# Optimization experiments

Measured on AMD Instinct MI355X. Metric: run time of the kernel, lower is better.

The kernel has to match this reference:

```python
import jax, jax.numpy as jnp
import numpy as np

N, S, D = 8, 1024, 512      # batch, seq_len, in_dim
H, KD, VD, OD = 8, 64, 64, 512  # heads, key_dim, value_dim, out_dim
GRAPH_WEIGHT = 0.5
NEG_INF = float('-inf')


def setup_inputs() -> dict:
    key = jax.random.key(0)
    ks = jax.random.split(key, 9)
    return {
        "x":    jax.random.normal(ks[0], (N, S, D), jnp.float32),
        "Wk":   jax.random.normal(ks[1], (H, D, KD), jnp.float32) * 0.02,
        "bk":   jax.random.normal(ks[2], (H, KD), jnp.float32) * 0.02,
        "Wv":   jax.random.normal(ks[3], (H, D, VD), jnp.float32) * 0.02,
        "bv":   jax.random.normal(ks[4], (H, VD), jnp.float32) * 0.02,
        "Wout": jax.random.normal(ks[5], (H * VD, OD), jnp.float32) * 0.02,
        "bout": jax.random.normal(ks[6], (OD,), jnp.float32) * 0.02,
        "graph": jax.random.normal(ks[7], (S, S), jnp.float32),
        "knn": 64,
    }


def reference(x, Wk, bk, Wv, bv, Wout, bout, graph, knn):
    # Per-head key/value projections (heads vectorized on leading axis h).
    k = jnp.einsum('nsd,hdk->hnsk', x, Wk) + bk[:, None, None, :]   # (H,N,S,KD)
    v = jnp.einsum('nsd,hdv->hnsv', x, Wv) + bv[:, None, None, :]   # (H,N,S,VD)
    q = k  # self-attention: query = key

    # att_unnorm = (q . k) / sqrt(key_dim)  -> (H,N,S,S)
    att = jnp.einsum('hnqk,hntk->hnqt', q, k) / np.sqrt(KD).astype(np.float32)

    # Causal mask (equivalent to the Python loop att[:, i, i+1:] = -inf).
    causal = jnp.tril(jnp.ones((S, S), dtype=bool))
    att = jnp.where(causal, att, NEG_INF)

    # knn top-k pooling: keep top-knn entries along the last axis, rest -> -inf.
    topv = jax.lax.top_k(att, knn)[0]                  # (H,N,S,knn)
    kth = topv[..., -1:]                               # kth largest per row
    att = jnp.where(att >= kth, att, NEG_INF)

    p = jax.nn.softmax(att, axis=-1)

    # Graph-weighted attention blend (graph is row-softmaxed at init time).
    att_graph = jax.nn.softmax(graph, axis=-1)         # (S,S)
    p = GRAPH_WEIGHT * att_graph + (1.0 - GRAPH_WEIGHT) * p

    # y_h = att @ value, then concat heads and output projection.
    y = jnp.einsum('hnqt,hntv->hnqv', p, v)            # (H,N,S,VD)
    y = y.transpose(1, 2, 0, 3).reshape(N, S, H * VD)  # head-major concat
    return y @ Wout + bout
```

## Files before the change

kernel.cpp:

```cpp
#include <hip/hip_runtime.h>
#include <math.h>

#define NB 8
#define SL 1024
#define DI 512
#define HH 8
#define KDN 64
#define VDN 64
#define ODN 512
#define ATT_SCALE 0.125f

#define KLO_OFF 2097152u
#define V_OFF   4194304u
#define G_OFF   8388608u
#define Y_OFF   9437184u

#define ORD_NEG_INF 0x007FFFFFu

typedef __attribute__((ext_vector_type(8))) short bf16x8;
typedef __attribute__((ext_vector_type(4))) float f32x4;

__device__ __forceinline__ unsigned fordu(float f) {
  unsigned b = __float_as_uint(f);
  return b ^ ((b & 0x80000000u) ? 0xFFFFFFFFu : 0x80000000u);
}
__device__ __forceinline__ float ifordu(unsigned k) {
  unsigned b = k ^ ((k & 0x80000000u) ? 0x80000000u : 0xFFFFFFFFu);
  return __uint_as_float(b);
}
__device__ __forceinline__ unsigned short f2bf(float f) {
  unsigned u = __float_as_uint(f);
  unsigned r = (u + 0x7FFFu + ((u >> 16) & 1u)) >> 16;
  return (unsigned short)r;
}
__device__ __forceinline__ float bf2f(unsigned short h) {
  return __uint_as_float(((unsigned)h) << 16);
}

__global__ __launch_bounds__(256) void kvproj_kernel(
    const float* __restrict__ x, const float* __restrict__ Wk, const float* __restrict__ bk,
    const float* __restrict__ Wv, const float* __restrict__ bv, float* __restrict__ ws)
{
  __shared__ float xs[64][68];
  __shared__ float wks[64][68];
  __shared__ float wvs[64][68];
  const int tid = threadIdx.x;
  const int tx = tid & 15, ty = tid >> 4;
  const int m0 = blockIdx.x * 64;
  const int h = blockIdx.y;
  const float* wkb = Wk + (size_t)h * (DI * KDN);
  const float* wvb = Wv + (size_t)h * (DI * VDN);
  float ak[4][4] = {{0.f}};
  float av[4][4] = {{0.f}};
  for (int dt = 0; dt < DI / 64; ++dt) {
    __syncthreads();
#pragma unroll
    for (int it = 0; it < 4; ++it) {
      const int r = ty + it * 16;
      const int c = tx * 4;
      *(float4*)&xs[r][c]  = *(const float4*)&x[(size_t)(m0 + r) * DI + dt * 64 + c];
      *(float4*)&wks[r][c] = *(const float4*)&wkb[(size_t)(dt * 64 + r) * KDN + c];
      *(float4*)&wvs[r][c] = *(const float4*)&wvb[(size_t)(dt * 64 + r) * VDN + c];
    }
    __syncthreads();
#pragma unroll 4
    for (int dd = 0; dd < 64; ++dd) {
      float a[4];
#pragma unroll
      for (int i = 0; i < 4; ++i) a[i] = xs[ty * 4 + i][dd];
      const float4 bkv = *(const float4*)&wks[dd][tx * 4];
      const float4 bvv = *(const float4*)&wvs[dd][tx * 4];
      const float bkj[4] = {bkv.x, bkv.y, bkv.z, bkv.w};
      const float bvj[4] = {bvv.x, bvv.y, bvv.z, bvv.w};
#pragma unroll
      for (int i = 0; i < 4; ++i) {
#pragma unroll
        for (int j = 0; j < 4; ++j) {
          ak[i][j] = __fmaf_rn(a[i], bkj[j], ak[i][j]);
          av[i][j] = __fmaf_rn(a[i], bvj[j], av[i][j]);
        }
      }
    }
  }
  const int n = m0 >> 10;
  const int s0 = m0 & 1023;
  float* vb = ws + V_OFF;
  unsigned short* khi = (unsigned short*)ws;
  unsigned short* klo = (unsigned short*)(ws + KLO_OFF);
#pragma unroll
  for (int i = 0; i < 4; ++i) {
    const int s = s0 + ty * 4 + i;
    float4 vv;
    vv.x = av[i][0] + bv[h * VDN + tx * 4 + 0];
    vv.y = av[i][1] + bv[h * VDN + tx * 4 + 1];
    vv.z = av[i][2] + bv[h * VDN + tx * 4 + 2];
    vv.w = av[i][3] + bv[h * VDN + tx * 4 + 3];
    *(float4*)&vb[((size_t)(h * NB + n) * SL + s) * VDN + tx * 4] = vv;
    union { unsigned short u[4]; uint2 v2; } ph, pl;
#pragma unroll
    for (int j = 0; j < 4; ++j) {
      const float kf = ak[i][j] + bk[h * KDN + tx * 4 + j];
      const unsigned short h16 = f2bf(kf);
      ph.u[j] = h16;
      pl.u[j] = f2bf(kf - bf2f(h16));
    }
    const size_t koff = ((size_t)(h * NB + n) * SL + s) * KDN + tx * 4;
    *(uint2*)&khi[koff] = ph.v2;
    *(uint2*)&klo[koff] = pl.v2;
  }
}

__global__ __launch_bounds__(256) void gsoftmax_kernel(const float* __restrict__ gin, float* __restrict__ ws)
{
  float* gout = ws + G_OFF;
  const int row = blockIdx.x;
  const int tid = threadIdx.x;
  const int lane = tid & 63, wave = tid >> 6;
  __shared__ float red[4];
  __shared__ float red2[4];
  float v[4];
  float m = -INFINITY;
#pragma unroll
  for (int i = 0; i < 4; ++i) {
    v[i] = gin[(size_t)row * SL + tid + i * 256];
    m = fmaxf(m, v[i]);
  }
#pragma unroll
  for (int off = 32; off; off >>= 1) m = fmaxf(m, __shfl_xor(m, off));
  if (lane == 0) red[wave] = m;
  __syncthreads();
  m = fmaxf(fmaxf(red[0], red[1]), fmaxf(red[2], red[3]));
  float e[4];
  float s = 0.f;
#pragma unroll
  for (int i = 0; i < 4; ++i) { e[i] = __expf(v[i] - m); s += e[i]; }
#pragma unroll
  for (int off = 32; off; off >>= 1) s += __shfl_xor(s, off);
  if (lane == 0) red2[wave] = s;
  __syncthreads();
  s = red2[0] + red2[1] + red2[2] + red2[3];
  const float inv = 1.0f / s;
#pragma unroll
  for (int i = 0; i < 4; ++i) gout[(size_t)row * SL + tid + i * 256] = e[i] * inv;
}

__global__ __launch_bounds__(256, 4) void attn_kernel(float* __restrict__ ws, const int* __restrict__ knn_p)
{
  __shared__ float S[16][260];
  const int tid = threadIdx.x;
  const int lane = tid & 63;
  const int wave = tid >> 6;
  const int q0 = blockIdx.x * 16;
  const int hn = blockIdx.y;
  const int h = hn >> 3, n = hn & 7;
  const int K = knn_p[0];
  const unsigned short* khi = (const unsigned short*)ws + (size_t)hn * SL * KDN;
  const unsigned short* klo = (const unsigned short*)(ws + KLO_OFF) + (size_t)hn * SL * KDN;
  const float* vb = ws + V_OFF + (size_t)hn * (SL * VDN);
  float* y = ws + Y_OFF;

  const int col = lane & 15, grp = lane >> 4;
  const bf16x8 a0h = *(const bf16x8*)&khi[(size_t)(q0 + col) * KDN + grp * 8];
  const bf16x8 a1h = *(const bf16x8*)&khi[(size_t)(q0 + col) * KDN + 32 + grp * 8];
  const bf16x8 a0l = *(const bf16x8*)&klo[(size_t)(q0 + col) * KDN + grp * 8];
  const bf16x8 a1l = *(const bf16x8*)&klo[(size_t)(q0 + col) * KDN + 32 + grp * 8];

  const int T = q0 / 16 + 1;
  const int rbase = wave * 4;

  float ev[4][8][2];
#pragma unroll
  for (int rr = 0; rr < 4; ++rr)
#pragma unroll
    for (int c = 0; c < 8; ++c) {
      ev[rr][c][0] = __uint_as_float(ORD_NEG_INF);
      ev[rr][c][1] = __uint_as_float(ORD_NEG_INF);
    }

#pragma unroll
  for (int ph = 0; ph < 4; ++ph) {
    const int tlo = ph * 16;
    const int thi = (T < tlo + 16) ? T : (tlo + 16);
    if (thi > tlo) {
      __syncthreads();
      for (int ti = tlo + wave; ti < thi; ti += 4) {
        const int t0 = ti * 16;
        const size_t bo = (size_t)(t0 + col) * KDN + grp * 8;
        const bf16x8 b0h = *(const bf16x8*)&khi[bo];
        const bf16x8 b1h = *(const bf16x8*)&khi[bo + 32];
        const bf16x8 b0l = *(const bf16x8*)&klo[bo];
        const bf16x8 b1l = *(const bf16x8*)&klo[bo + 32];
        f32x4 d = {0.f, 0.f, 0.f, 0.f};
        d = __builtin_amdgcn_mfma_f32_16x16x32_bf16(a0h, b0h, d, 0, 0, 0);
        d = __builtin_amdgcn_mfma_f32_16x16x32_bf16(a1h, b1h, d, 0, 0, 0);
        d = __builtin_amdgcn_mfma_f32_16x16x32_bf16(a0h, b0l, d, 0, 0, 0);
        d = __builtin_amdgcn_mfma_f32_16x16x32_bf16(a1h, b1l, d, 0, 0, 0);
        d = __builtin_amdgcn_mfma_f32_16x16x32_bf16(a0l, b0h, d, 0, 0, 0);
        d = __builtin_amdgcn_mfma_f32_16x16x32_bf16(a1l, b1h, d, 0, 0, 0);
        d = __builtin_amdgcn_mfma_f32_16x16x32_bf16(a0l, b0l, d, 0, 0, 0);
        d = __builtin_amdgcn_mfma_f32_16x16x32_bf16(a1l, b1l, d, 0, 0, 0);
        const int tl = t0 - ph * 256 + col;
#pragma unroll
        for (int r = 0; r < 4; ++r) S[grp * 4 + r][tl] = d[r];
      }
      __syncthreads();
#pragma unroll
      for (int rr = 0; rr < 4; ++rr) {
        const int q = q0 + rbase + rr;
        const int cmr = q >> 7;
#pragma unroll
        for (int cc = 0; cc < 2; ++cc) {
          const int c = ph * 2 + cc;
          if (c <= cmr) {
            const float2 sv = *(const float2*)&S[rbase + rr][cc * 128 + lane * 2];
            const int t0 = c * 128 + lane * 2;
            const unsigned k0 = (t0     <= q) ? fordu(sv.x * ATT_SCALE) : ORD_NEG_INF;
            const unsigned k1 = (t0 + 1 <= q) ? fordu(sv.y * ATT_SCALE) : ORD_NEG_INF;
            ev[rr][c][0] = __uint_as_float(k0);
            ev[rr][c][1] = __uint_as_float(k1);
          }
        }
      }
    }
  }
  __syncthreads();

  float* elist = (float*)((char*)&S[0][0] + wave * 768);
  unsigned short* tlist = (unsigned short*)(elist + 128);

#pragma unroll
  for (int rr = 0; rr < 4; ++rr) {
    const int q = q0 + rbase + rr;

    unsigned u[16];
#pragma unroll
    for (int c = 0; c < 8; ++c) {
      u[c * 2]     = __float_as_uint(ev[rr][c][0]);
      u[c * 2 + 1] = __float_as_uint(ev[rr][c][1]);
    }

    unsigned lmax = u[0];
#pragma unroll
    for (int i = 1; i < 16; ++i) lmax = lmax > u[i] ? lmax : u[i];
    unsigned mk = lmax, t0k = lmax;
#pragma unroll
    for (int off = 32; off; off >>= 1) {
      const unsigned om = (unsigned)__shfl_xor((int)mk, off);
      const unsigned ot = (unsigned)__shfl_xor((int)t0k, off);
      mk = mk > om ? mk : om;
      t0k = t0k < ot ? t0k : ot;
    }
    const float m = ifordu(mk);

    unsigned kth;
    if (q < K) {
      kth = ORD_NEG_INF;
    } else {
      unsigned lo = (K <= 64) ? t0k : 0u;
      unsigned hi = mk;
      while (lo < hi) {
        const unsigned mid = lo + ((hi - lo + 1) >> 1);
        int cnt = 0;
#pragma unroll
        for (int i = 0; i < 16; ++i)
          cnt += (int)__popcll(__ballot(u[i] >= mid));
        if (cnt >= K) lo = mid; else hi = mid - 1;
      }
      kth = lo;
    }

    float Z = 0.f;
#pragma unroll
    for (int c = 0; c < 8; ++c) {
#pragma unroll
      for (int j = 0; j < 2; ++j) {
        const unsigned k = u[c * 2 + j];
        float e = 0.f;
        if (k >= kth) e = __expf(ifordu(k) - m);
        ev[rr][c][j] = e;
        Z += e;
      }
    }
#pragma unroll
    for (int off = 32; off; off >>= 1) Z += __shfl_xor(Z, off);

    const unsigned long long lt = (1ull << lane) - 1ull;
    int cnt = 0;
#pragma unroll
    for (int c = 0; c < 8; ++c) {
#pragma unroll
      for (int j = 0; j < 2; ++j) {
        const float e = ev[rr][c][j];
        const unsigned long long msk = __ballot(e > 0.f);
        if (e > 0.f) {
          const int pos = cnt + (int)__popcll(msk & lt);
          if (pos < 128) {
            elist[pos] = e;
            tlist[pos] = (unsigned short)(c * 128 + lane * 2 + j);
          }
        }
        cnt += (int)__popcll(msk);
      }
    }
    cnt = (cnt < 128) ? cnt : 128;

    float yacc = 0.f;
    int i2 = 0;
    for (; i2 + 4 <= cnt; i2 += 4) {
      const float4 e4 = *(const float4*)&elist[i2];
      const ushort4 t4 = *(const ushort4*)&tlist[i2];
      yacc = __fmaf_rn(e4.x, vb[(size_t)t4.x * VDN + lane], yacc);
      yacc = __fmaf_rn(e4.y, vb[(size_t)t4.y * VDN + lane], yacc);
      yacc = __fmaf_rn(e4.z, vb[(size_t)t4.z * VDN + lane], yacc);
      yacc = __fmaf_rn(e4.w, vb[(size_t)t4.w * VDN + lane], yacc);
    }
    for (; i2 < cnt; ++i2) {
      yacc = __fmaf_rn(elist[i2], vb[(size_t)tlist[i2] * VDN + lane], yacc);
    }
    y[((size_t)(n * SL + q)) * ODN + h * VDN + lane] = yacc * (0.5f / Z);
  }
}

__global__ __launch_bounds__(256) void gv_kernel(float* __restrict__ ws)
{
  __shared__ float as_[64][68];
  __shared__ float bs_[64][68];
  const int tid = threadIdx.x;
  const int tx = tid & 15, ty = tid >> 4;
  const int q0 = blockIdx.x * 64;
  const int hn = blockIdx.y;
  const int h = hn >> 3, n = hn & 7;
  const float* g = ws + G_OFF;
  const float* vb = ws + V_OFF + (size_t)hn * (SL * VDN);
  float* y = ws + Y_OFF;
  float acc[4][4] = {{0.f}};
  for (int kt = 0; kt < 16; ++kt) {
    __syncthreads();
#pragma unroll
    for (int it = 0; it < 4; ++it) {
      const int r = ty + it * 16;
      const int c = tx * 4;
      *(float4*)&as_[r][c] = *(const float4*)&g[(size_t)(q0 + r) * SL + kt * 64 + c];
      *(float4*)&bs_[r][c] = *(const float4*)&vb[(size_t)(kt * 64 + r) * VDN + c];
    }
    __syncthreads();
#pragma unroll 4
    for (int dd = 0; dd < 64; ++dd) {
      float a[4];
#pragma unroll
      for (int i = 0; i < 4; ++i) a[i] = as_[ty * 4 + i][dd];
      const float4 b4 = *(const float4*)&bs_[dd][tx * 4];
      const float bj[4] = {b4.x, b4.y, b4.z, b4.w};
#pragma unroll
      for (int i = 0; i < 4; ++i)
#pragma unroll
        for (int j = 0; j < 4; ++j)
          acc[i][j] = __fmaf_rn(a[i], bj[j], acc[i][j]);
    }
  }
#pragma unroll
  for (int i = 0; i < 4; ++i) {
    const size_t off = ((size_t)(n * SL + q0 + ty * 4 + i)) * ODN + h * VDN + tx * 4;
    float4 cur = *(float4*)&y[off];
    cur.x += 0.5f * acc[i][0];
    cur.y += 0.5f * acc[i][1];
    cur.z += 0.5f * acc[i][2];
    cur.w += 0.5f * acc[i][3];
    *(float4*)&y[off] = cur;
  }
}

__global__ __launch_bounds__(256) void wtprep_kernel(const float* __restrict__ Wout, float* __restrict__ ws)
{
  __shared__ float tile[64][65];
  unsigned short* wth = (unsigned short*)ws;
  unsigned short* wtl = wth + ODN * ODN;
  const int t = threadIdx.x;
  const int od0 = blockIdx.x * 64;
  const int k0 = blockIdx.y * 64;
  const int r = t >> 2, c4 = (t & 3) * 16;
#pragma unroll
  for (int j = 0; j < 4; ++j) {
    *(float4*)&tile[r][c4 + j * 4] = *(const float4*)&Wout[(size_t)(k0 + r) * ODN + od0 + c4 + j * 4];
  }
  __syncthreads();
  union { unsigned short u[16]; uint4 v[2]; } hi, lo;
#pragma unroll
  for (int j = 0; j < 16; ++j) {
    const float f = tile[c4 + j][r];
    const unsigned short h16 = f2bf(f);
    hi.u[j] = h16;
    lo.u[j] = f2bf(f - bf2f(h16));
  }
  const size_t o = (size_t)(od0 + r) * ODN + k0 + c4;
  *(uint4*)&wth[o] = hi.v[0];
  *(uint4*)&wth[o + 8] = hi.v[1];
  *(uint4*)&wtl[o] = lo.v[0];
  *(uint4*)&wtl[o + 8] = lo.v[1];
}

__global__ __launch_bounds__(256) void out_kernel(
    const float* __restrict__ bout, const float* __restrict__ ws, float* __restrict__ out)
{
  const unsigned short* wth = (const unsigned short*)ws;
  const unsigned short* wtl = wth + ODN * ODN;
  const float* y = ws + Y_OFF;
  const int tid = threadIdx.x;
  const int lane = tid & 63;
  const int wave = tid >> 6;
  const int col = lane & 15, grp = lane >> 4;
  const int od0 = blockIdx.x * 64;
  const int m0 = blockIdx.y * 64 + wave * 16;

  f32x4 acc[4];
#pragma unroll
  for (int odt = 0; odt < 4; ++odt) acc[odt] = (f32x4){0.f, 0.f, 0.f, 0.f};

  const float* yrow = y + (size_t)(m0 + col) * ODN + grp * 8;
  for (int ks = 0; ks < 16; ++ks) {
    const float4 ya = *(const float4*)&yrow[ks * 32];
    const float4 yb = *(const float4*)&yrow[ks * 32 + 4];
    union { unsigned short u[8]; bf16x8 v; } ah, al;
    const float yf[8] = {ya.x, ya.y, ya.z, ya.w, yb.x, yb.y, yb.z, yb.w};
#pragma unroll
    for (int j = 0; j < 8; ++j) {
      const unsigned short h16 = f2bf(yf[j]);
      ah.u[j] = h16;
      al.u[j] = f2bf(yf[j] - bf2f(h16));
    }
#pragma unroll
    for (int odt = 0; odt < 4; ++odt) {
      const size_t bo = (size_t)(od0 + odt * 16 + col) * ODN + ks * 32 + grp * 8;
      const bf16x8 bh = *(const bf16x8*)&wth[bo];
      const bf16x8 bl = *(const bf16x8*)&wtl[bo];
      acc[odt] = __builtin_amdgcn_mfma_f32_16x16x32_bf16(ah.v, bh, acc[odt], 0, 0, 0);
      acc[odt] = __builtin_amdgcn_mfma_f32_16x16x32_bf16(ah.v, bl, acc[odt], 0, 0, 0);
      acc[odt] = __builtin_amdgcn_mfma_f32_16x16x32_bf16(al.v, bh, acc[odt], 0, 0, 0);
    }
  }

#pragma unroll
  for (int odt = 0; odt < 4; ++odt) {
    const int od = od0 + odt * 16 + col;
    const float bo = bout[od];
#pragma unroll
    for (int r = 0; r < 4; ++r) {
      out[(size_t)(m0 + grp * 4 + r) * ODN + od] = acc[odt][r] + bo;
    }
  }
}

extern "C" void kernel_launch(void* const* d_in, const int* in_sizes, int n_in,
                              void* d_out, int out_size, void* d_ws, size_t ws_size,
                              hipStream_t stream)
{
  const float* x     = (const float*)d_in[0];
  const float* Wk    = (const float*)d_in[1];
  const float* bk    = (const float*)d_in[2];
  const float* Wv    = (const float*)d_in[3];
  const float* bv    = (const float*)d_in[4];
  const float* Wout  = (const float*)d_in[5];
  const float* bout  = (const float*)d_in[6];
  const float* graph = (const float*)d_in[7];
  const int*   knn   = (const int*)d_in[8];
  float* out = (float*)d_out;
  float* ws  = (float*)d_ws;

  kvproj_kernel<<<dim3(128, 8), 256, 0, stream>>>(x, Wk, bk, Wv, bv, ws);
  gsoftmax_kernel<<<dim3(1024), 256, 0, stream>>>(graph, ws);
  attn_kernel<<<dim3(64, 64), 256, 0, stream>>>(ws, knn);
  wtprep_kernel<<<dim3(8, 8), 256, 0, stream>>>(Wout, ws);
  gv_kernel<<<dim3(16, 64), 256, 0, stream>>>(ws);
  out_kernel<<<dim3(8, 128), 256, 0, stream>>>(bout, ws, out);
}
```

Before: 604.0 us.

## Move KV projection and graph-value GEMM to split-bf16 MFMA

The fp32 scalar-FMA GEMMs in kvproj and gv are replaced with bf16x3 split-precision MFMA (hi*hi + hi*lo + lo*hi). New prep kernels split x, Wk/Wv, the graph softmax and a transposed V into hi/lo bf16 halves, and workspace regions are reused and remapped, with wtprep moved after gv. The aim is to use matrix cores for these GEMMs in exchange for extra launches, conversion traffic and slightly lower precision. Output stores become scalar, and LDS tiling is dropped in favour of direct global loads.

```diff
diff --git a/kernel.cpp b/kernel.cpp
--- a/kernel.cpp
+++ b/kernel.cpp
@@ -37,82 +37,124 @@
   return __uint_as_float(((unsigned)h) << 16);
 }
 
+__global__ __launch_bounds__(256) void xprep_kernel(const float* __restrict__ x, float* __restrict__ ws)
+{
+  unsigned short* xhi = (unsigned short*)(ws + Y_OFF);
+  unsigned short* xlo = xhi + (size_t)NB * SL * DI;
+  const size_t i = (size_t)blockIdx.x * 256 + threadIdx.x;
+  const float4 v = *(const float4*)&x[i * 4];
+  const float vf[4] = {v.x, v.y, v.z, v.w};
+  union { unsigned short u[4]; uint2 v2; } hi, lo;
+#pragma unroll
+  for (int j = 0; j < 4; ++j) {
+    const unsigned short h16 = f2bf(vf[j]);
+    hi.u[j] = h16;
+    lo.u[j] = f2bf(vf[j] - bf2f(h16));
+  }
+  *(uint2*)&xhi[i * 4] = hi.v2;
+  *(uint2*)&xlo[i * 4] = lo.v2;
+}
+
+__global__ __launch_bounds__(256) void wprep_kernel(
+    const float* __restrict__ Wk, const float* __restrict__ Wv, float* __restrict__ ws)
+{
+  __shared__ float tile[64][65];
+  unsigned short* gbase = (unsigned short*)(ws + G_OFF);
+  const int t = threadIdx.x;
+  const int d0 = blockIdx.x * 64;
+  const int hs = blockIdx.y;
+  const int h = hs & 7, which = hs >> 3;
+  const float* W = (which == 0) ? (Wk + (size_t)h * DI * KDN) : (Wv + (size_t)h * DI * VDN);
+  unsigned short* whi = gbase + (size_t)which * 524288 + (size_t)h * KDN * DI;
+  unsigned short* wlo = whi + 262144;
+  const int r = t >> 2, c4 = (t & 3) * 16;
+#pragma unroll
+  for (int j = 0; j < 4; ++j)
+    *(float4*)&tile[r][c4 + j * 4] = *(const float4*)&W[(size_t)(d0 + r) * KDN + c4 + j * 4];
+  __syncthreads();
+  union { unsigned short u[16]; uint4 v[2]; } hi, lo;
+#pragma unroll
+  for (int j = 0; j < 16; ++j) {
+    const float f = tile[c4 + j][r];
+    const unsigned short h16 = f2bf(f);
+    hi.u[j] = h16;
+    lo.u[j] = f2bf(f - bf2f(h16));
+  }
+  const size_t o = (size_t)r * DI + d0 + c4;
+  *(uint4*)&whi[o] = hi.v[0];
+  *(uint4*)&whi[o + 8] = hi.v[1];
+  *(uint4*)&wlo[o] = lo.v[0];
+  *(uint4*)&wlo[o + 8] = lo.v[1];
+}
+
 __global__ __launch_bounds__(256) void kvproj_kernel(
-    const float* __restrict__ x, const float* __restrict__ Wk, const float* __restrict__ bk,
-    const float* __restrict__ Wv, const float* __restrict__ bv, float* __restrict__ ws)
-{
-  __shared__ float xs[64][68];
-  __shared__ float wks[64][68];
-  __shared__ float wvs[64][68];
+    const float* __restrict__ bk, const float* __restrict__ bv, float* __restrict__ ws)
+{
+  const unsigned short* xhi = (const unsigned short*)(ws + Y_OFF);
+  const unsigned short* xlo = xhi + (size_t)NB * SL * DI;
+  const unsigned short* gbase = (const unsigned short*)(ws + G_OFF);
+  const unsigned short* wkthi = gbase;
+  const unsigned short* wktlo = gbase + 262144;
+  const unsigned short* wvthi = gbase + 524288;
+  const unsigned short* wvtlo = gbase + 786432;
+  unsigned short* khi = (unsigned short*)ws;
+  unsigned short* klo = (unsigned short*)(ws + KLO_OFF);
+  float* vb = ws + V_OFF;
+
   const int tid = threadIdx.x;
-  const int tx = tid & 15, ty = tid >> 4;
+  const int lane = tid & 63;
+  const int wave = tid >> 6;
+  const int col = lane & 15, grp = lane >> 4;
   const int m0 = blockIdx.x * 64;
   const int h = blockIdx.y;
-  const float* wkb = Wk + (size_t)h * (DI * KDN);
-  const float* wvb = Wv + (size_t)h * (DI * VDN);
-  float ak[4][4] = {{0.f}};
-  float av[4][4] = {{0.f}};
-  for (int dt = 0; dt < DI / 64; ++dt) {
-    __syncthreads();
-#pragma unroll
-    for (int it = 0; it < 4; ++it) {
-      const int r = ty + it * 16;
-      const int c = tx * 4;
-      *(float4*)&xs[r][c]  = *(const float4*)&x[(size_t)(m0 + r) * DI + dt * 64 + c];
-      *(float4*)&wks[r][c] = *(const float4*)&wkb[(size_t)(dt * 64 + r) * KDN + c];
-      *(float4*)&wvs[r][c] = *(const float4*)&wvb[(size_t)(dt * 64 + r) * VDN + c];
-    }
-    __syncthreads();
-#pragma unroll 4
-    for (int dd = 0; dd < 64; ++dd) {
-      float a[4];
-#pragma unroll
-      for (int i = 0; i < 4; ++i) a[i] = xs[ty * 4 + i][dd];
-      const float4 bkv = *(const float4*)&wks[dd][tx * 4];
-      const float4 bvv = *(const float4*)&wvs[dd][tx * 4];
-      const float bkj[4] = {bkv.x, bkv.y, bkv.z, bkv.w};
-      const float bvj[4] = {bvv.x, bvv.y, bvv.z, bvv.w};
-#pragma unroll
-      for (int i = 0; i < 4; ++i) {
-#pragma unroll
-        for (int j = 0; j < 4; ++j) {
-          ak[i][j] = __fmaf_rn(a[i], bkj[j], ak[i][j]);
-          av[i][j] = __fmaf_rn(a[i], bvj[j], av[i][j]);
-        }
-      }
-    }
-  }
-  const int n = m0 >> 10;
-  const int s0 = m0 & 1023;
-  float* vb = ws + V_OFF;
-  unsigned short* khi = (unsigned short*)ws;
-  unsigned short* klo = (unsigned short*)(ws + KLO_OFF);
-#pragma unroll
-  for (int i = 0; i < 4; ++i) {
-    const int s = s0 + ty * 4 + i;
-    float4 vv;
-    vv.x = av[i][0] + bv[h * VDN + tx * 4 + 0];
-    vv.y = av[i][1] + bv[h * VDN + tx * 4 + 1];
-    vv.z = av[i][2] + bv[h * VDN + tx * 4 + 2];
-    vv.w = av[i][3] + bv[h * VDN + tx * 4 + 3];
-    *(float4*)&vb[((size_t)(h * NB + n) * SL + s) * VDN + tx * 4] = vv;
-    union { unsigned short u[4]; uint2 v2; } ph, pl;
-#pragma unroll
-    for (int j = 0; j < 4; ++j) {
-      const float kf = ak[i][j] + bk[h * KDN + tx * 4 + j];
+  const int n = m0 >> 10, s0 = m0 & 1023;
+
+  f32x4 ack[4], acv[4];
+#pragma unroll
+  for (int odt = 0; odt < 4; ++odt) { ack[odt] = (f32x4){0,0,0,0}; acv[odt] = (f32x4){0,0,0,0}; }
+
+  const size_t arow = (size_t)(m0 + wave * 16 + col) * DI;
+  for (int ks = 0; ks < 16; ++ks) {
+    const bf16x8 ah = *(const bf16x8*)&xhi[arow + ks * 32 + grp * 8];
+    const bf16x8 al = *(const bf16x8*)&xlo[arow + ks * 32 + grp * 8];
+#pragma unroll
+    for (int odt = 0; odt < 4; ++odt) {
+      const size_t bo = (size_t)(h * 64 + odt * 16 + col) * DI + ks * 32 + grp * 8;
+      const bf16x8 kh = *(const bf16x8*)&wkthi[bo];
+      const bf16x8 kl = *(const bf16x8*)&wktlo[bo];
+      ack[odt] = __builtin_amdgcn_mfma_f32_16x16x32_bf16(ah, kh, ack[odt], 0, 0, 0);
+      ack[odt] = __builtin_amdgcn_mfma_f32_16x16x32_bf16(ah, kl, ack[odt], 0, 0, 0);
+      ack[odt] = __builtin_amdgcn_mfma_f32_16x16x32_bf16(al, kh, ack[odt], 0, 0, 0);
+      const bf16x8 vh = *(const bf16x8*)&wvthi[bo];
+      const bf16x8 vl = *(const bf16x8*)&wvtlo[bo];
+      acv[odt] = __builtin_amdgcn_mfma_f32_16x16x32_bf16(ah, vh, acv[odt], 0, 0, 0);
+      acv[odt] = __builtin_amdgcn_mfma_f32_16x16x32_bf16(ah, vl, acv[odt], 0, 0, 0);
+      acv[odt] = __builtin_amdgcn_mfma_f32_16x16x32_bf16(al, vh, acv[odt], 0, 0, 0);
+    }
+  }
+
+  const size_t hnbase = ((size_t)(h * NB + n) * SL);
+#pragma unroll
+  for (int odt = 0; odt < 4; ++odt) {
+    const int kd = odt * 16 + col;
+    const float bkv = bk[h * KDN + kd];
+    const float bvv = bv[h * VDN + kd];
+#pragma unroll
+    for (int r = 0; r < 4; ++r) {
+      const int s = s0 + wave * 16 + grp * 4 + r;
+      const float kf = ack[odt][r] + bkv;
       const unsigned short h16 = f2bf(kf);
-      ph.u[j] = h16;
-      pl.u[j] = f2bf(kf - bf2f(h16));
-    }
-    const size_t koff = ((size_t)(h * NB + n) * SL + s) * KDN + tx * 4;
-    *(uint2*)&khi[koff] = ph.v2;
-    *(uint2*)&klo[koff] = pl.v2;
+      khi[(hnbase + s) * KDN + kd] = h16;
+      klo[(hnbase + s) * KDN + kd] = f2bf(kf - bf2f(h16));
+      vb[(hnbase + s) * VDN + kd] = acv[odt][r] + bvv;
+    }
   }
 }
 
 __global__ __launch_bounds__(256) void gsoftmax_kernel(const float* __restrict__ gin, float* __restrict__ ws)
 {
-  float* gout = ws + G_OFF;
+  unsigned short* ghi = (unsigned short*)(ws + G_OFF);
+  unsigned short* glo = ghi + (size_t)SL * SL;
   const int row = blockIdx.x;
   const int tid = threadIdx.x;
   const int lane = tid & 63, wave = tid >> 6;
@@ -141,7 +183,12 @@
   s = red2[0] + red2[1] + red2[2] + red2[3];
   const float inv = 1.0f / s;
 #pragma unroll
-  for (int i = 0; i < 4; ++i) gout[(size_t)row * SL + tid + i * 256] = e[i] * inv;
+  for (int i = 0; i < 4; ++i) {
+    const float p = e[i] * inv;
+    const unsigned short h16 = f2bf(p);
+    ghi[(size_t)row * SL + tid + i * 256] = h16;
+    glo[(size_t)row * SL + tid + i * 256] = f2bf(p - bf2f(h16));
+  }
 }
 
 __global__ __launch_bounds__(256, 4) void attn_kernel(float* __restrict__ ws, const int* __restrict__ knn_p)
@@ -321,59 +368,84 @@
   }
 }
 
+__global__ __launch_bounds__(256) void vtprep_kernel(float* __restrict__ ws)
+{
+  __shared__ float tile[64][65];
+  const int t = threadIdx.x;
+  const int t0 = blockIdx.x * 64;
+  const int hn = blockIdx.y;
+  const float* vb = ws + V_OFF + (size_t)hn * (SL * VDN);
+  unsigned short* vthi = (unsigned short*)ws + (size_t)hn * VDN * SL;
+  unsigned short* vtlo = (unsigned short*)(ws + KLO_OFF) + (size_t)hn * VDN * SL;
+  const int r = t >> 2, c4 = (t & 3) * 16;
+#pragma unroll
+  for (int j = 0; j < 4; ++j)
+    *(float4*)&tile[r][c4 + j * 4] = *(const float4*)&vb[(size_t)(t0 + r) * VDN + c4 + j * 4];
+  __syncthreads();
+  union { unsigned short u[16]; uint4 v[2]; } hi, lo;
+#pragma unroll
+  for (int j = 0; j < 16; ++j) {
+    const float f = tile[c4 + j][r];
+    const unsigned short h16 = f2bf(f);
+    hi.u[j] = h16;
+    lo.u[j] = f2bf(f - bf2f(h16));
+  }
+  const size_t o = (size_t)r * SL + t0 + c4;
+  *(uint4*)&vthi[o] = hi.v[0];
+  *(uint4*)&vthi[o + 8] = hi.v[1];
+  *(uint4*)&vtlo[o] = lo.v[0];
+  *(uint4*)&vtlo[o + 8] = lo.v[1];
+}
+
 __global__ __launch_bounds__(256) void gv_kernel(float* __restrict__ ws)
 {
-  __shared__ float as_[64][68];
-  __shared__ float bs_[64][68];
+  const unsigned short* ghi = (const unsigned short*)(ws + G_OFF);
+  const unsigned short* glo = ghi + (size_t)SL * SL;
   const int tid = threadIdx.x;
-  const int tx = tid & 15, ty = tid >> 4;
+  const int lane = tid & 63;
+  const int wave = tid >> 6;
+  const int col = lane & 15, grp = lane >> 4;
   const int q0 = blockIdx.x * 64;
   const int hn = blockIdx.y;
   const int h = hn >> 3, n = hn & 7;
-  const float* g = ws + G_OFF;
-  const float* vb = ws + V_OFF + (size_t)hn * (SL * VDN);
+  const unsigned short* vthi = (const unsigned short*)ws + (size_t)hn * VDN * SL;
+  const unsigned short* vtlo = (const unsigned short*)(ws + KLO_OFF) + (size_t)hn * VDN * SL;
   float* y = ws + Y_OFF;
-  float acc[4][4] = {{0.f}};
-  for (int kt = 0; kt < 16; ++kt) {
-    __syncthreads();
-#pragma unroll
-    for (int it = 0; it < 4; ++it) {
-      const int r = ty + it * 16;
-      const int c = tx * 4;
-      *(float4*)&as_[r][c] = *(const float4*)&g[(size_t)(q0 + r) * SL + kt * 64 + c];
-      *(float4*)&bs_[r][c] = *(const float4*)&vb[(size_t)(kt * 64 + r) * VDN + c];
-    }
-    __syncthreads();
-#pragma unroll 4
-    for (int dd = 0; dd < 64; ++dd) {
-      float a[4];
-#pragma unroll
-      for (int i = 0; i < 4; ++i) a[i] = as_[ty * 4 + i][dd];
-      const float4 b4 = *(const float4*)&bs_[dd][tx * 4];
-      const float bj[4] = {b4.x, b4.y, b4.z, b4.w};
-#pragma unroll
-      for (int i = 0; i < 4; ++i)
-#pragma unroll
-        for (int j = 0; j < 4; ++j)
-          acc[i][j] = __fmaf_rn(a[i], bj[j], acc[i][j]);
-    }
-  }
-#pragma unroll
-  for (int i = 0; i < 4; ++i) {
-    const size_t off = ((size_t)(n * SL + q0 + ty * 4 + i)) * ODN + h * VDN + tx * 4;
-    float4 cur = *(float4*)&y[off];
-    cur.x += 0.5f * acc[i][0];
-    cur.y += 0.5f * acc[i][1];
-    cur.z += 0.5f * acc[i][2];
-    cur.w += 0.5f * acc[i][3];
-    *(float4*)&y[off] = cur;
+
+  f32x4 acc[4];
+#pragma unroll
+  for (int odt = 0; odt < 4; ++odt) acc[odt] = (f32x4){0,0,0,0};
+
+  const size_t arow = (size_t)(q0 + wave * 16 + col) * SL;
+  for (int ks = 0; ks < 32; ++ks) {
+    const bf16x8 ah = *(const bf16x8*)&ghi[arow + ks * 32 + grp * 8];
+    const bf16x8 al = *(const bf16x8*)&glo[arow + ks * 32 + grp * 8];
+#pragma unroll
+    for (int odt = 0; odt < 4; ++odt) {
+      const size_t bo = (size_t)(odt * 16 + col) * SL + ks * 32 + grp * 8;
+      const bf16x8 bh = *(const bf16x8*)&vthi[bo];
+      const bf16x8 bl = *(const bf16x8*)&vtlo[bo];
+      acc[odt] = __builtin_amdgcn_mfma_f32_16x16x32_bf16(ah, bh, acc[odt], 0, 0, 0);
+      acc[odt] = __builtin_amdgcn_mfma_f32_16x16x32_bf16(ah, bl, acc[odt], 0, 0, 0);
+      acc[odt] = __builtin_amdgcn_mfma_f32_16x16x32_bf16(al, bh, acc[odt], 0, 0, 0);
+    }
+  }
+
+#pragma unroll
+  for (int odt = 0; odt < 4; ++odt) {
+    const int vd = odt * 16 + col;
+#pragma unroll
+    for (int r = 0; r < 4; ++r) {
+      const size_t off = ((size_t)(n * SL + q0 + wave * 16 + grp * 4 + r)) * ODN + h * VDN + vd;
+      y[off] += 0.5f * acc[odt][r];
+    }
   }
 }
 
 __global__ __launch_bounds__(256) void wtprep_kernel(const float* __restrict__ Wout, float* __restrict__ ws)
 {
   __shared__ float tile[64][65];
-  unsigned short* wth = (unsigned short*)ws;
+  unsigned short* wth = (unsigned short*)(ws + G_OFF);
   unsigned short* wtl = wth + ODN * ODN;
   const int t = threadIdx.x;
   const int od0 = blockIdx.x * 64;
@@ -402,7 +474,7 @@
 __global__ __launch_bounds__(256) void out_kernel(
     const float* __restrict__ bout, const float* __restrict__ ws, float* __restrict__ out)
 {
-  const unsigned short* wth = (const unsigned short*)ws;
+  const unsigned short* wth = (const unsigned short*)(ws + G_OFF);
   const unsigned short* wtl = wth + ODN * ODN;
   const float* y = ws + Y_OFF;
   const int tid = threadIdx.x;
@@ -466,10 +538,13 @@
   float* out = (float*)d_out;
   float* ws  = (float*)d_ws;
 
-  kvproj_kernel<<<dim3(128, 8), 256, 0, stream>>>(x, Wk, bk, Wv, bv, ws);
+  xprep_kernel<<<dim3(4096), 256, 0, stream>>>(x, ws);
+  wprep_kernel<<<dim3(8, 16), 256, 0, stream>>>(Wk, Wv, ws);
+  kvproj_kernel<<<dim3(128, 8), 256, 0, stream>>>(bk, bv, ws);
   gsoftmax_kernel<<<dim3(1024), 256, 0, stream>>>(graph, ws);
   attn_kernel<<<dim3(64, 64), 256, 0, stream>>>(ws, knn);
+  vtprep_kernel<<<dim3(16, 64), 256, 0, stream>>>(ws);
+  gv_kernel<<<dim3(16, 64), 256, 0, stream>>>(ws);
   wtprep_kernel<<<dim3(8, 8), 256, 0, stream>>>(Wout, ws);
-  gv_kernel<<<dim3(16, 64), 256, 0, stream>>>(ws);
   out_kernel<<<dim3(8, 128), 256, 0, stream>>>(bout, ws, out);
 }
```

Result: slower. 675.1 us (+11.8%).
